# Kernel tuning notes

Hardware: AMD Instinct MI355X
Metric: run time of the kernel (lower is better)

Reference implementation:

```python
import jax, jax.numpy as jnp
import numpy as np

B = 512; S = 2048; K = 128; E = 64; A = 128; H = 4; DK = A // H; OD = 64; BITS = 32
FOH = 15; FMH = 4; FSP = 4; LSP = 50
VOH = 10001; VMH = 100001; VSP = 10001
D0 = 27 * E


def _short_attn(tgt, seq, mask, qW, qb, kW, kb, vW, vb, oW, ob):
    # tgt [F,b,1,E], seq [F,b,s,E], mask [F,b,1,s] bool
    F_, b_, s_, _ = seq.shape
    q = (jnp.einsum('fbte,fea->fbta', tgt, qW) + qb[:, None, None, :]).reshape(F_, b_, -1, H, DK)
    k = (jnp.einsum('fbse,fea->fbsa', seq, kW) + kb[:, None, None, :]).reshape(F_, b_, s_, H, DK)
    v = (jnp.einsum('fbse,fea->fbsa', seq, vW) + vb[:, None, None, :]).reshape(F_, b_, s_, H, DK)
    scores = jnp.einsum('fbthd,fbshd->fbhts', q, k) / (DK ** 0.5)
    scores = jnp.where(mask[:, :, None, :, :], scores, -jnp.inf)
    attn = jax.nn.softmax(scores, axis=-1)
    out = jnp.einsum('fbhts,fbshd->fbthd', attn, v).reshape(F_, b_, -1, A)
    return jnp.einsum('fbta,fao->fbto', out, oW) + ob[:, None, None, :]  # [F,b,1,OD]


def _forward(one_hot_tables, multi_hot_tables, special_tables, hash_weights,
             sqW, sqb, skW, skb, svW, svb, soW, sob,
             lqW, lqb, lkW, lkb, lvW, lvb, loW, lob,
             W0, b0, W1, b1, W2, b2, outW, outb,
             one_hot_ids, multi_hot_ids, special_ids):
    lookup = jax.vmap(lambda t, i: t[i], in_axes=(0, 0))
    oh_emb = jax.vmap(lambda t, i: t[i], in_axes=(0, 1))(one_hot_tables, one_hot_ids)  # [FOH,B,E]
    mh_mask = multi_hot_ids >= 0                                                       # [FMH,B,S]
    mh_emb = lookup(multi_hot_tables, jnp.where(mh_mask, multi_hot_ids, 0))            # [FMH,B,S,E]
    sp_mask = special_ids >= 0
    sp_emb = (lookup(special_tables, jnp.where(sp_mask, special_ids, 0))
              * sp_mask[..., None].astype(jnp.float32)).sum(axis=2)                    # [FSP,B,E] sum combiner
    tgt = oh_emb[:FMH][:, :, None, :]  # targets = first 4 one-hot fields, [4,B,1,E]
    # short attention over first K candidates of each history
    short = _short_attn(tgt, mh_emb[:, :, :K, :], mh_mask[:, :, None, :K],
                        sqW, sqb, skW, skb, svW, svb, soW, sob)                        # [4,B,1,OD]
    # long attention: LSH hash -> hamming-sim topk -> gather -> attention
    th = (jnp.einsum('fbe,eh->fbh', tgt[:, :, 0, :], hash_weights) > 0).astype(jnp.float32)
    sh = (jnp.einsum('fbse,eh->fbsh', mh_emb, hash_weights) > 0).astype(jnp.float32)
    sim = -jnp.sum(jnp.abs(sh - th[:, :, None, :]), axis=-1)                           # [4,B,S]
    sim = jnp.where(mh_mask, sim, -jnp.inf)
    _, idx = jax.lax.top_k(sim, K)                                                     # [4,B,K]
    topk_seq = jnp.take_along_axis(mh_emb, idx[..., None], axis=2)                     # [4,B,K,E]
    topk_mask = jnp.take_along_axis(mh_mask, idx, axis=2)[:, :, None, :]
    long = _short_attn(tgt, topk_seq, topk_mask,
                       lqW, lqb, lkW, lkb, lvW, lvb, loW, lob)                         # [4,B,1,OD]
    b_ = oh_emb.shape[1]
    feats = jnp.concatenate([
        oh_emb.transpose(1, 0, 2).reshape(b_, -1),
        sp_emb.transpose(1, 0, 2).reshape(b_, -1),
        short[:, :, 0, :].transpose(1, 0, 2).reshape(b_, -1),
        long[:, :, 0, :].transpose(1, 0, 2).reshape(b_, -1)], axis=-1)                 # [B, 27*E]
    x = jax.nn.relu(feats @ W0 + b0)
    x = jax.nn.relu(x @ W1 + b1)
    x = jax.nn.relu(x @ W2 + b2)
    logits = (x @ outW + outb)[:, 0]
    return jax.nn.sigmoid(logits), logits


def setup_inputs():
    ks = list(jax.random.split(jax.random.key(0), 64))
    def nrm(shape, scale):
        return jax.random.normal(ks.pop(), shape, dtype=jnp.float32) * scale
    std = (2.0 / 512.0) ** 0.5
    d = {}
    d['one_hot_tables'] = nrm((FOH, VOH, E), std)
    d['multi_hot_tables'] = nrm((FMH, VMH, E), std)
    d['special_tables'] = nrm((FSP, VSP, E), std)
    d['hash_weights'] = nrm((E, BITS), 1.0)
    for p in ('s', 'l'):
        d[p + 'qW'] = nrm((FMH, E, A), E ** -0.5); d[p + 'qb'] = nrm((FMH, A), 0.01)
        d[p + 'kW'] = nrm((FMH, E, A), E ** -0.5); d[p + 'kb'] = nrm((FMH, A), 0.01)
        d[p + 'vW'] = nrm((FMH, E, A), E ** -0.5); d[p + 'vb'] = nrm((FMH, A), 0.01)
        d[p + 'oW'] = nrm((FMH, A, OD), A ** -0.5); d[p + 'ob'] = nrm((FMH, OD), 0.01)
    dims = [D0, 1024, 512, 256]
    for i in range(3):
        d['W%d' % i] = nrm((dims[i], dims[i + 1]), dims[i] ** -0.5)
        d['b%d' % i] = nrm((dims[i + 1],), 0.01)
    d['outW'] = nrm((256, 1), 256 ** -0.5)
    d['outb'] = nrm((1,), 0.01)
    d['one_hot_ids'] = jax.random.randint(ks.pop(), (B, FOH), 0, VOH, dtype=jnp.int32)
    d['multi_hot_ids'] = jax.random.randint(ks.pop(), (FMH, B, S), 0, VMH, dtype=jnp.int32)
    d['special_ids'] = jax.random.randint(ks.pop(), (FSP, B, LSP), 0, VSP, dtype=jnp.int32)
    return d


def reference(one_hot_tables, multi_hot_tables, special_tables, hash_weights, sqW, sqb, skW, skb, svW, svb, soW, sob, lqW, lqb, lkW, lkb, lvW, lvb, loW, lob, W0, b0, W1, b1, W2, b2, outW, outb, one_hot_ids, multi_hot_ids, special_ids):
    return _forward(one_hot_tables, multi_hot_tables, special_tables, hash_weights,
                    sqW, sqb, skW, skb, svW, svb, soW, sob,
                    lqW, lqb, lkW, lkb, lvW, lvb, loW, lob,
                    W0, b0, W1, b1, W2, b2, outW, outb,
                    one_hot_ids, multi_hot_ids, special_ids)
```

## Files before the change

### kernel.cpp

```cpp
#include <hip/hip_runtime.h>
#include <math.h>

#define F_MH 4
#define NB   512
#define SEQ  2048
#define TOPK 128
#define EDIM 64
#define ADIM 128
#define VOH  10001
#define VMH  100001
#define NROWS (F_MH * VMH)
#define D0   1728
#define RSQRT32 0.17677669529663687f

typedef __bf16 bf16x8 __attribute__((ext_vector_type(8)));
typedef __bf16 bf16x4 __attribute__((ext_vector_type(4)));
typedef float  f32x4  __attribute__((ext_vector_type(4)));

__global__ __launch_bounds__(256) void k_hash(const float* __restrict__ tab,
                                              const float* __restrict__ hw,
                                              unsigned int* __restrict__ sig)
{
    const int t = threadIdx.x;
    const int base = blockIdx.x * 1024 + t;
    const float4* __restrict__ hw4 = (const float4*)hw;
    float4 acc[4][8];
#pragma unroll
    for (int i = 0; i < 4; ++i)
#pragma unroll
        for (int h = 0; h < 8; ++h) acc[i][h] = make_float4(0.f, 0.f, 0.f, 0.f);
    int r[4];
    const float4* rp[4];
#pragma unroll
    for (int i = 0; i < 4; ++i) {
        int rr = base + i * 256;
        r[i] = rr;
        rr = (rr < NROWS) ? rr : 0;
        rp[i] = (const float4*)(tab + (size_t)rr * 64);
    }
    for (int e4 = 0; e4 < 16; ++e4) {
        float4 x[4];
#pragma unroll
        for (int i = 0; i < 4; ++i) x[i] = rp[i][e4];
#pragma unroll
        for (int j = 0; j < 4; ++j) {
            const int e = e4 * 4 + j;
#pragma unroll
            for (int h = 0; h < 8; ++h) {
                const float4 w = hw4[e * 8 + h];
#pragma unroll
                for (int i = 0; i < 4; ++i) {
                    const float xs = (j == 0) ? x[i].x : (j == 1) ? x[i].y
                                   : (j == 2) ? x[i].z : x[i].w;
                    acc[i][h].x += xs * w.x; acc[i][h].y += xs * w.y;
                    acc[i][h].z += xs * w.z; acc[i][h].w += xs * w.w;
                }
            }
        }
    }
#pragma unroll
    for (int i = 0; i < 4; ++i) {
        unsigned int bits = 0u;
#pragma unroll
        for (int h = 0; h < 8; ++h) {
            bits |= (acc[i][h].x > 0.f ? 1u : 0u) << (h * 4);
            bits |= (acc[i][h].y > 0.f ? 2u : 0u) << (h * 4);
            bits |= (acc[i][h].z > 0.f ? 4u : 0u) << (h * 4);
            bits |= (acc[i][h].w > 0.f ? 8u : 0u) << (h * 4);
        }
        if (r[i] < NROWS) sig[r[i]] = bits;
    }
}

__global__ __launch_bounds__(256) void k_topk(const float* __restrict__ oh_tab,
                                              const float* __restrict__ hw,
                                              const unsigned int* __restrict__ sig,
                                              const int* __restrict__ oh_ids,
                                              const int* __restrict__ mh_ids,
                                              int* __restrict__ sel)
{
    const int b = blockIdx.x, f = blockIdx.y, t = threadIdx.x;
    __shared__ float tgt[64];
    __shared__ unsigned int thbits;
    __shared__ int hist[34];
    __shared__ int c_lt[256], c_eq[256];
    __shared__ int s_dstar, s_cntlt;
    if (t < 64) tgt[t] = oh_tab[((size_t)f * VOH + oh_ids[b * 15 + f]) * 64 + t];
    if (t == 0) thbits = 0u;
    if (t < 34) hist[t] = 0;
    __syncthreads();
    if (t < 32) {
        float acc = 0.f;
#pragma unroll
        for (int e = 0; e < 64; ++e) acc += tgt[e] * hw[e * 32 + t];
        if (acc > 0.f) atomicOr(&thbits, 1u << t);
    }
    __syncthreads();
    const unsigned int th = thbits;
    const int* idp = mh_ids + (size_t)(f * NB + b) * SEQ + t * 8;
    int ids[8], dv[8];
#pragma unroll
    for (int j = 0; j < 8; ++j) {
        int id = idp[j];
        ids[j] = id;
        int d = (id >= 0) ? __popc(sig[f * VMH + id] ^ th) : 33;
        dv[j] = d;
        atomicAdd(&hist[d], 1);
    }
    __syncthreads();
    if (t == 0) {
        int cum = 0, ds = 33, cl = 0;
        for (int d = 0; d <= 33; ++d) {
            if (cum + hist[d] >= TOPK) { ds = d; cl = cum; break; }
            cum += hist[d];
        }
        s_dstar = ds; s_cntlt = cl;
    }
    __syncthreads();
    const int Dstar = s_dstar, cntlt = s_cntlt;
    int nlt = 0, neq = 0;
#pragma unroll
    for (int j = 0; j < 8; ++j) {
        nlt += (dv[j] < Dstar);
        neq += (dv[j] == Dstar);
    }
    c_lt[t] = nlt; c_eq[t] = neq;
    __syncthreads();
    for (int off = 1; off < 256; off <<= 1) {
        int vl = 0, ve = 0;
        if (t >= off) { vl = c_lt[t - off]; ve = c_eq[t - off]; }
        __syncthreads();
        c_lt[t] += vl; c_eq[t] += ve;
        __syncthreads();
    }
    int lt_pos = c_lt[t] - nlt;
    int eq_pos = cntlt + c_eq[t] - neq;
    int* selp = sel + (size_t)(f * NB + b) * TOPK;
#pragma unroll
    for (int j = 0; j < 8; ++j) {
        if (dv[j] < Dstar) { selp[lt_pos++] = ids[j]; }
        else if (dv[j] == Dstar) {
            if (eq_pos < TOPK) selp[eq_pos] = ids[j];
            eq_pos++;
        }
    }
}

__global__ __launch_bounds__(256) void k_attn(const float* __restrict__ oh_tab,
                                              const float* __restrict__ mh_tab,
                                              const int* __restrict__ oh_ids,
                                              const int* __restrict__ mh_ids,
                                              const int* __restrict__ sel,
                                              const float* __restrict__ sqW, const float* __restrict__ sqb,
                                              const float* __restrict__ skW, const float* __restrict__ skb,
                                              const float* __restrict__ svW, const float* __restrict__ svb,
                                              const float* __restrict__ soW, const float* __restrict__ sob,
                                              const float* __restrict__ lqW, const float* __restrict__ lqb,
                                              const float* __restrict__ lkW, const float* __restrict__ lkb,
                                              const float* __restrict__ lvW, const float* __restrict__ lvb,
                                              const float* __restrict__ loW, const float* __restrict__ lob,
                                              __bf16* __restrict__ feats)
{
    const int b = blockIdx.x, f = blockIdx.y, z = blockIdx.z, t = threadIdx.x;
    const float* WQ = (z ? lqW : sqW) + (size_t)f * (EDIM * ADIM);
    const float* bq = (z ? lqb : sqb) + f * ADIM;
    const float* WK = (z ? lkW : skW) + (size_t)f * (EDIM * ADIM);
    const float* bk = (z ? lkb : skb) + f * ADIM;
    const float* WV = (z ? lvW : svW) + (size_t)f * (EDIM * ADIM);
    const float* bv = (z ? lvb : svb) + f * ADIM;
    const float* WO = (z ? loW : soW) + (size_t)f * (ADIM * 64);
    const float* bo = (z ? lob : sob) + f * 64;

    __shared__ float tgt[64];
    __shared__ int   sid[128];
    __shared__ float seqT[64][132];
    __shared__ float qv[128];
    __shared__ float qk[4][64];
    __shared__ float qkb4[4];
    __shared__ float sc[4][128];
    __shared__ float wemb[4][64];
    __shared__ float outv[128];

    if (t < 64) tgt[t] = oh_tab[((size_t)f * VOH + oh_ids[b * 15 + f]) * 64 + t];
    if (t < 128) {
        int id;
        if (z == 0) id = mh_ids[(size_t)(f * NB + b) * SEQ + t];
        else        id = sel[(size_t)(f * NB + b) * TOPK + t];
        sid[t] = id;
    }
    __syncthreads();
#pragma unroll
    for (int i = 0; i < 8; ++i) {
        int v = t + i * 256;
        int row = v >> 4, c4 = (v & 15) << 2;
        int id = sid[row];
        float4 ev = make_float4(0.f, 0.f, 0.f, 0.f);
        if (id >= 0) ev = *(const float4*)&mh_tab[((size_t)f * VMH + id) * 64 + c4];
        seqT[c4 + 0][row] = ev.x; seqT[c4 + 1][row] = ev.y;
        seqT[c4 + 2][row] = ev.z; seqT[c4 + 3][row] = ev.w;
    }
    if (t < 128) {
        float acc = bq[t];
#pragma unroll
        for (int e = 0; e < 64; ++e) acc += tgt[e] * WQ[e * 128 + t];
        qv[t] = acc;
    }
    __syncthreads();
    {
        const int h = t >> 6, e = t & 63;
        float acc = 0.f;
#pragma unroll
        for (int d = 0; d < 32; ++d) acc += qv[h * 32 + d] * WK[e * 128 + h * 32 + d];
        qk[h][e] = acc * RSQRT32;
    }
    if (t < 4) {
        float acc = 0.f;
#pragma unroll
        for (int d = 0; d < 32; ++d) acc += qv[t * 32 + d] * bk[t * 32 + d];
        qkb4[t] = acc * RSQRT32;
    }
    __syncthreads();
#pragma unroll
    for (int rep = 0; rep < 2; ++rep) {
        int idx = t + rep * 256;
        int h = idx >> 7, s = idx & 127;
        float acc = qkb4[h];
#pragma unroll
        for (int e4 = 0; e4 < 16; ++e4) {
            float4 q4 = *(const float4*)&qk[h][e4 * 4];
            acc += seqT[e4 * 4 + 0][s] * q4.x + seqT[e4 * 4 + 1][s] * q4.y
                 + seqT[e4 * 4 + 2][s] * q4.z + seqT[e4 * 4 + 3][s] * q4.w;
        }
        sc[h][s] = (sid[s] >= 0) ? acc : -INFINITY;
    }
    __syncthreads();
    {
        const int h = t >> 6, l = t & 63;
        float v0 = sc[h][l], v1 = sc[h][l + 64];
        float m = fmaxf(v0, v1);
        for (int off = 32; off; off >>= 1) m = fmaxf(m, __shfl_xor(m, off));
        float p0 = expf(v0 - m), p1 = expf(v1 - m);
        float ssum = p0 + p1;
        for (int off = 32; off; off >>= 1) ssum += __shfl_xor(ssum, off);
        float inv = 1.f / ssum;
        sc[h][l] = p0 * inv; sc[h][l + 64] = p1 * inv;
    }
    __syncthreads();
    {
        const int h = t >> 6, e = t & 63;
        float acc = 0.f;
#pragma unroll
        for (int s4 = 0; s4 < 32; ++s4) {
            float4 a4 = *(const float4*)&sc[h][s4 * 4];
            float4 e4 = *(const float4*)&seqT[e][s4 * 4];
            acc += a4.x * e4.x + a4.y * e4.y + a4.z * e4.z + a4.w * e4.w;
        }
        wemb[h][e] = acc;
    }
    __syncthreads();
    if (t < 128) {
        const int h = t >> 5;
        float acc = bv[t];
#pragma unroll
        for (int e = 0; e < 64; ++e) acc += wemb[h][e] * WV[e * 128 + t];
        outv[t] = acc;
    }
    __syncthreads();
    if (t < 64) {
        float acc = bo[t];
#pragma unroll
        for (int a = 0; a < 128; ++a) acc += outv[a] * WO[a * 64 + t];
        feats[(size_t)b * D0 + (z ? 1472 : 1216) + f * 64 + t] = (__bf16)acc;
    }
}

__global__ __launch_bounds__(256) void k_feats(const float* __restrict__ oh_tab,
                                               const float* __restrict__ sp_tab,
                                               const int* __restrict__ oh_ids,
                                               const int* __restrict__ sp_ids,
                                               __bf16* __restrict__ feats)
{
    const int b = blockIdx.x, t = threadIdx.x;
    __shared__ int sidl[200];
    __shared__ int ohid[15];
    if (t < 200) sidl[t] = sp_ids[(size_t)((t / 50) * NB + b) * 50 + (t % 50)];
    if (t >= 240 && t < 255) ohid[t - 240] = oh_ids[b * 15 + (t - 240)];
    __syncthreads();
    __bf16* fr = feats + (size_t)b * D0;
    for (int p = t; p < 960; p += 256) {
        int f = p >> 6, e = p & 63;
        fr[p] = (__bf16)oh_tab[((size_t)f * VOH + ohid[f]) * 64 + e];
    }
    {
        int f = t >> 6, e = t & 63;
        float acc = 0.f;
        for (int j = 0; j < 50; ++j) {
            int id = sidl[f * 50 + j];
            if (id >= 0) acc += sp_tab[((size_t)f * VOH + id) * 64 + e];
        }
        fr[960 + t] = (__bf16)acc;
    }
}

__global__ __launch_bounds__(256) void k_trans(const float* __restrict__ W,
                                               __bf16* __restrict__ WT,
                                               int K, int N)
{
    __shared__ float tile[32][33];
    const int t = threadIdx.x;
    const int n0 = blockIdx.x * 32, k0 = blockIdx.y * 32;
    const int c = t & 31, r = t >> 5;
#pragma unroll
    for (int i = 0; i < 4; ++i)
        tile[r + 8 * i][c] = W[(size_t)(k0 + r + 8 * i) * N + n0 + c];
    __syncthreads();
#pragma unroll
    for (int i = 0; i < 4; ++i)
        WT[(size_t)(n0 + r + 8 * i) * K + k0 + c] = (__bf16)tile[c][r + 8 * i];
}

__global__ __launch_bounds__(256) void gemm_mfma(const __bf16* __restrict__ A,
                                                 const __bf16* __restrict__ BT,
                                                 const float* __restrict__ bias,
                                                 __bf16* __restrict__ C,
                                                 int M, int N, int K, int relu)
{
    __shared__ __bf16 As[64][72];
    __shared__ __bf16 Bs[64][72];
    const int t = threadIdx.x;
    const int n0 = blockIdx.x * 64, m0 = blockIdx.y * 64;
    const int wave = t >> 6, lane = t & 63;
    const int wm = (wave >> 1) * 32, wn = (wave & 1) * 32;
    const int row16 = lane & 15, quad = lane >> 4;
    f32x4 acc[2][2] = {};
    const int sr = t >> 3;
    const int sseg = (t & 7) * 8;
    for (int k0 = 0; k0 < K; k0 += 64) {
        bf16x8 av0 = *(const bf16x8*)&A[(size_t)(m0 + sr) * K + k0 + sseg];
        bf16x8 av1 = *(const bf16x8*)&A[(size_t)(m0 + sr + 32) * K + k0 + sseg];
        bf16x8 bv0 = *(const bf16x8*)&BT[(size_t)(n0 + sr) * K + k0 + sseg];
        bf16x8 bv1 = *(const bf16x8*)&BT[(size_t)(n0 + sr + 32) * K + k0 + sseg];
        __syncthreads();
        *(bf16x8*)&As[sr][sseg] = av0;
        *(bf16x8*)&As[sr + 32][sseg] = av1;
        *(bf16x8*)&Bs[sr][sseg] = bv0;
        *(bf16x8*)&Bs[sr + 32][sseg] = bv1;
        __syncthreads();
#pragma unroll
        for (int kk = 0; kk < 2; ++kk) {
            bf16x8 a0 = *(const bf16x8*)&As[wm + row16][kk * 32 + quad * 8];
            bf16x8 a1 = *(const bf16x8*)&As[wm + 16 + row16][kk * 32 + quad * 8];
            bf16x8 b0 = *(const bf16x8*)&Bs[wn + row16][kk * 32 + quad * 8];
            bf16x8 b1 = *(const bf16x8*)&Bs[wn + 16 + row16][kk * 32 + quad * 8];
            acc[0][0] = __builtin_amdgcn_mfma_f32_16x16x32_bf16(a0, b0, acc[0][0], 0, 0, 0);
            acc[0][1] = __builtin_amdgcn_mfma_f32_16x16x32_bf16(a0, b1, acc[0][1], 0, 0, 0);
            acc[1][0] = __builtin_amdgcn_mfma_f32_16x16x32_bf16(a1, b0, acc[1][0], 0, 0, 0);
            acc[1][1] = __builtin_amdgcn_mfma_f32_16x16x32_bf16(a1, b1, acc[1][1], 0, 0, 0);
        }
    }
#pragma unroll
    for (int i = 0; i < 2; ++i)
#pragma unroll
        for (int j = 0; j < 2; ++j) {
            const int col = n0 + wn + j * 16 + row16;
            const float bz = bias[col];
#pragma unroll
            for (int r = 0; r < 4; ++r) {
                const int rowm = m0 + wm + i * 16 + quad * 4 + r;
                float v = acc[i][j][r] + bz;
                if (relu) v = fmaxf(v, 0.f);
                C[(size_t)rowm * N + col] = (__bf16)v;
            }
        }
}

__global__ __launch_bounds__(256) void k_out(const __bf16* __restrict__ x2,
                                             const float* __restrict__ outW,
                                             const float* __restrict__ outb,
                                             float* __restrict__ out)
{
    const int t = threadIdx.x;
    const int wave = t >> 6, lane = t & 63;
    const int row = blockIdx.x * 4 + wave;
    bf16x4 xv = *(const bf16x4*)&x2[(size_t)row * 256 + lane * 4];
    const float4 wv = *(const float4*)&outW[lane * 4];
    float v = (float)xv[0] * wv.x + (float)xv[1] * wv.y
            + (float)xv[2] * wv.z + (float)xv[3] * wv.w;
    for (int off = 32; off; off >>= 1) v += __shfl_down(v, off);
    if (lane == 0) {
        float lg = v + outb[0];
        out[row] = 1.f / (1.f + expf(-lg));
        out[NB + row] = lg;
    }
}

extern "C" void kernel_launch(void* const* d_in, const int* in_sizes, int n_in,
                              void* d_out, int out_size, void* d_ws, size_t ws_size,
                              hipStream_t stream)
{
    const float* oh_tab = (const float*)d_in[0];
    const float* mh_tab = (const float*)d_in[1];
    const float* sp_tab = (const float*)d_in[2];
    const float* hw     = (const float*)d_in[3];
    const float* sqW = (const float*)d_in[4];  const float* sqb = (const float*)d_in[5];
    const float* skW = (const float*)d_in[6];  const float* skb = (const float*)d_in[7];
    const float* svW = (const float*)d_in[8];  const float* svb = (const float*)d_in[9];
    const float* soW = (const float*)d_in[10]; const float* sob = (const float*)d_in[11];
    const float* lqW = (const float*)d_in[12]; const float* lqb = (const float*)d_in[13];
    const float* lkW = (const float*)d_in[14]; const float* lkb = (const float*)d_in[15];
    const float* lvW = (const float*)d_in[16]; const float* lvb = (const float*)d_in[17];
    const float* loW = (const float*)d_in[18]; const float* lob = (const float*)d_in[19];
    const float* W0 = (const float*)d_in[20];  const float* b0 = (const float*)d_in[21];
    const float* W1 = (const float*)d_in[22];  const float* b1 = (const float*)d_in[23];
    const float* W2 = (const float*)d_in[24];  const float* b2 = (const float*)d_in[25];
    const float* outW = (const float*)d_in[26]; const float* outb = (const float*)d_in[27];
    const int* oh_ids = (const int*)d_in[28];
    const int* mh_ids = (const int*)d_in[29];
    const int* sp_ids = (const int*)d_in[30];

    char* ws = (char*)d_ws;
    unsigned int* sig = (unsigned int*)(ws + 0);
    int*    sel   = (int*)   (ws + 1600512);
    __bf16* feats = (__bf16*)(ws + 2649088);
    __bf16* x0    = (__bf16*)(ws + 4418560);
    __bf16* x1    = (__bf16*)(ws + 5467136);
    __bf16* x2    = (__bf16*)(ws + 5991424);
    __bf16* WT0   = (__bf16*)(ws + 6253568);
    __bf16* WT1   = (__bf16*)(ws + 9792512);
    __bf16* WT2   = (__bf16*)(ws + 10841088);

    k_trans<<<dim3(1024 / 32, 1728 / 32), 256, 0, stream>>>(W0, WT0, 1728, 1024);
    k_trans<<<dim3(512 / 32, 1024 / 32), 256, 0, stream>>>(W1, WT1, 1024, 512);
    k_trans<<<dim3(256 / 32, 512 / 32), 256, 0, stream>>>(W2, WT2, 512, 256);

    k_hash<<<(NROWS + 1023) / 1024, 256, 0, stream>>>(mh_tab, hw, sig);
    k_topk<<<dim3(NB, F_MH), 256, 0, stream>>>(oh_tab, hw, sig, oh_ids, mh_ids, sel);
    k_feats<<<NB, 256, 0, stream>>>(oh_tab, sp_tab, oh_ids, sp_ids, feats);
    k_attn<<<dim3(NB, F_MH, 2), 256, 0, stream>>>(oh_tab, mh_tab, oh_ids, mh_ids, sel,
                                                  sqW, sqb, skW, skb, svW, svb, soW, sob,
                                                  lqW, lqb, lkW, lkb, lvW, lvb, loW, lob,
                                                  feats);
    gemm_mfma<<<dim3(16, 8), 256, 0, stream>>>(feats, WT0, b0, x0, 512, 1024, 1728, 1);
    gemm_mfma<<<dim3(8, 8), 256, 0, stream>>>(x0, WT1, b1, x1, 512, 512, 1024, 1);
    gemm_mfma<<<dim3(4, 8), 256, 0, stream>>>(x1, WT2, b2, x2, 512, 256, 512, 1);
    k_out<<<NB / 4, 256, 0, stream>>>(x2, outW, outb, (float*)d_out);
}
```

Measured before the change: 493.7 us.

## Stage hash-table rows through LDS with coalesced loads, one row per thread

The LSH signature kernel now loads a 128-row tile of the multi-hot table into padded shared memory with coalesced float4 loads, and each thread then computes the 32 hash projections for one row. Before, each thread read four rows with strided per-row float4 loads, which coalesce poorly. The blocks are smaller (128 threads) and there are many more of them, and only 8 float4 accumulators are live instead of 32, which cuts register pressure. The cost is shared-memory traffic and a barrier, and each weight load now feeds one row instead of four.

```diff
diff --git a/kernel.cpp b/kernel.cpp
--- a/kernel.cpp
+++ b/kernel.cpp
@@ -17,59 +17,48 @@
 typedef __bf16 bf16x4 __attribute__((ext_vector_type(4)));
 typedef float  f32x4  __attribute__((ext_vector_type(4)));
 
-__global__ __launch_bounds__(256) void k_hash(const float* __restrict__ tab,
+__global__ __launch_bounds__(128) void k_hash(const float* __restrict__ tab,
                                               const float* __restrict__ hw,
                                               unsigned int* __restrict__ sig)
 {
+    __shared__ float rows[128][65];
     const int t = threadIdx.x;
-    const int base = blockIdx.x * 1024 + t;
     const float4* __restrict__ hw4 = (const float4*)hw;
-    float4 acc[4][8];
-#pragma unroll
-    for (int i = 0; i < 4; ++i)
-#pragma unroll
-        for (int h = 0; h < 8; ++h) acc[i][h] = make_float4(0.f, 0.f, 0.f, 0.f);
-    int r[4];
-    const float4* rp[4];
-#pragma unroll
-    for (int i = 0; i < 4; ++i) {
-        int rr = base + i * 256;
-        r[i] = rr;
-        rr = (rr < NROWS) ? rr : 0;
-        rp[i] = (const float4*)(tab + (size_t)rr * 64);
-    }
-    for (int e4 = 0; e4 < 16; ++e4) {
-        float4 x[4];
-#pragma unroll
-        for (int i = 0; i < 4; ++i) x[i] = rp[i][e4];
-#pragma unroll
-        for (int j = 0; j < 4; ++j) {
-            const int e = e4 * 4 + j;
-#pragma unroll
-            for (int h = 0; h < 8; ++h) {
-                const float4 w = hw4[e * 8 + h];
-#pragma unroll
-                for (int i = 0; i < 4; ++i) {
-                    const float xs = (j == 0) ? x[i].x : (j == 1) ? x[i].y
-                                   : (j == 2) ? x[i].z : x[i].w;
-                    acc[i][h].x += xs * w.x; acc[i][h].y += xs * w.y;
-                    acc[i][h].z += xs * w.z; acc[i][h].w += xs * w.w;
-                }
-            }
-        }
-    }
-#pragma unroll
-    for (int i = 0; i < 4; ++i) {
-        unsigned int bits = 0u;
+    const size_t blk_dw = (size_t)blockIdx.x * 8192;
+    const long long lim = (long long)NROWS * 64 - (long long)blk_dw;
+#pragma unroll
+    for (int i = 0; i < 16; ++i) {
+        const int idx = i * 512 + t * 4;
+        float4 v = make_float4(0.f, 0.f, 0.f, 0.f);
+        if (idx < lim) v = *(const float4*)(tab + blk_dw + idx);
+        const int row = idx >> 6, e = idx & 63;
+        rows[row][e + 0] = v.x; rows[row][e + 1] = v.y;
+        rows[row][e + 2] = v.z; rows[row][e + 3] = v.w;
+    }
+    __syncthreads();
+    float4 acc[8];
+#pragma unroll
+    for (int h = 0; h < 8; ++h) acc[h] = make_float4(0.f, 0.f, 0.f, 0.f);
+#pragma unroll 16
+    for (int e = 0; e < 64; ++e) {
+        const float x = rows[t][e];
 #pragma unroll
         for (int h = 0; h < 8; ++h) {
-            bits |= (acc[i][h].x > 0.f ? 1u : 0u) << (h * 4);
-            bits |= (acc[i][h].y > 0.f ? 2u : 0u) << (h * 4);
-            bits |= (acc[i][h].z > 0.f ? 4u : 0u) << (h * 4);
-            bits |= (acc[i][h].w > 0.f ? 8u : 0u) << (h * 4);
-        }
-        if (r[i] < NROWS) sig[r[i]] = bits;
-    }
+            const float4 w = hw4[e * 8 + h];
+            acc[h].x += x * w.x; acc[h].y += x * w.y;
+            acc[h].z += x * w.z; acc[h].w += x * w.w;
+        }
+    }
+    unsigned int bits = 0u;
+#pragma unroll
+    for (int h = 0; h < 8; ++h) {
+        bits |= (acc[h].x > 0.f ? 1u : 0u) << (h * 4);
+        bits |= (acc[h].y > 0.f ? 2u : 0u) << (h * 4);
+        bits |= (acc[h].z > 0.f ? 4u : 0u) << (h * 4);
+        bits |= (acc[h].w > 0.f ? 8u : 0u) << (h * 4);
+    }
+    const int r = blockIdx.x * 128 + t;
+    if (r < NROWS) sig[r] = bits;
 }
 
 __global__ __launch_bounds__(256) void k_topk(const float* __restrict__ oh_tab,
@@ -433,7 +422,7 @@
     k_trans<<<dim3(512 / 32, 1024 / 32), 256, 0, stream>>>(W1, WT1, 1024, 512);
     k_trans<<<dim3(256 / 32, 512 / 32), 256, 0, stream>>>(W2, WT2, 512, 256);
 
-    k_hash<<<(NROWS + 1023) / 1024, 256, 0, stream>>>(mh_tab, hw, sig);
+    k_hash<<<(NROWS + 127) / 128, 128, 0, stream>>>(mh_tab, hw, sig);
     k_topk<<<dim3(NB, F_MH), 256, 0, stream>>>(oh_tab, hw, sig, oh_ids, mh_ids, sel);
     k_feats<<<NB, 256, 0, stream>>>(oh_tab, sp_tab, oh_ids, sp_ids, feats);
     k_attn<<<dim3(NB, F_MH, 2), 256, 0, stream>>>(oh_tab, mh_tab, oh_ids, mh_ids, sel,
```

New measurement: 472.0 us. 1.05x faster.
